# Kernel tuning notes

Measured on AMD Instinct MI355X. Metric: run time of the kernel, lower is better.

Reference implementation:

```python
import jax, jax.numpy as jnp
import numpy as np
import math

D_MODEL = 1024
N_HEADS = 16
D_K = D_MODEL // N_HEADS
BSZ = 4
SEQ = 2048


def setup_inputs() -> dict:
    key = jax.random.key(0)
    ks = jax.random.split(key, 10)
    x = jax.random.normal(ks[0], (BSZ, SEQ, D_MODEL), dtype=jnp.float32)
    pad_mask = jnp.zeros((BSZ, 1, 1, SEQ), dtype=jnp.int32)
    s = 0.02
    Wq = jax.random.normal(ks[1], (D_MODEL, D_MODEL), jnp.float32) * s
    bq = jax.random.normal(ks[2], (D_MODEL,), jnp.float32) * s
    Wk = jax.random.normal(ks[3], (D_MODEL, D_MODEL), jnp.float32) * s
    bk = jax.random.normal(ks[4], (D_MODEL,), jnp.float32) * s
    Wv = jax.random.normal(ks[5], (D_MODEL, D_MODEL), jnp.float32) * s
    bv = jax.random.normal(ks[6], (D_MODEL,), jnp.float32) * s
    Wo = jax.random.normal(ks[7], (D_MODEL, D_MODEL), jnp.float32) * s
    bo = jax.random.normal(ks[8], (D_MODEL,), jnp.float32) * s
    return {"x": x, "pad_mask": pad_mask, "Wq": Wq, "bq": bq, "Wk": Wk,
            "bk": bk, "Wv": Wv, "bv": bv, "Wo": Wo, "bo": bo}


def reference(x, pad_mask, Wq, bq, Wk, bk, Wv, bv, Wo, bo):
    bsz, seq_len, d_model = x.shape
    h, dk = N_HEADS, D_K

    def split(W, b):
        # torch Linear: x @ W.T + b ; then [b,s,h,dk] -> [b,h,s,dk]
        y = jnp.einsum('bsd,ed->bse', x, W) + b
        return y.reshape(bsz, seq_len, h, dk).transpose(0, 2, 1, 3)

    q = split(Wq, bq)
    k = split(Wk, bk)
    v = split(Wv, bv)

    scores = jnp.einsum('bhqd,bhkd->bhqk', q, k) / math.sqrt(dk)
    causal = jnp.triu(jnp.ones((seq_len, seq_len), dtype=bool), k=1)
    scores = jnp.where(causal[None, None], -jnp.inf, scores)
    scores = jnp.where(pad_mask == 1, -jnp.inf, scores)
    attn = jax.nn.softmax(scores, axis=-1)
    attn = jnp.nan_to_num(attn, nan=0.0)
    out = jnp.einsum('bhqk,bhkd->bhqd', attn, v)
    out = out.transpose(0, 2, 1, 3).reshape(bsz, seq_len, d_model)
    # dropout is identity in eval mode
    return jnp.einsum('bsd,ed->bse', out, Wo) + bo
```

## Files before the change

kernel.cpp:

```cpp
#include <hip/hip_runtime.h>
#include <stdint.h>
#include <stddef.h>


typedef __bf16 bf16;
typedef __bf16 bf16x8 __attribute__((ext_vector_type(8)));
typedef __bf16 bf16x4 __attribute__((ext_vector_type(4)));
typedef float f32x4 __attribute__((ext_vector_type(4)));

#define DM   1024
#define NH   16
#define DK   64
#define BSZ  4
#define SEQL 2048
#define NTOK 8192
#define NEGB -3.0e38f

__device__ __forceinline__ void async16(const bf16* g, void* l) {
  __builtin_amdgcn_global_load_lds(
      (__attribute__((address_space(1))) void*)g,
      (__attribute__((address_space(3))) void*)l, 16, 0, 0);
}

__global__ __launch_bounds__(256) void cvt_all(
    const float* __restrict__ x,
    const float* __restrict__ w0, const float* __restrict__ w1,
    const float* __restrict__ w2, const float* __restrict__ w3,
    const int* __restrict__ pad,
    bf16* __restrict__ xd,
    bf16* __restrict__ d0, bf16* __restrict__ d1,
    bf16* __restrict__ d2, bf16* __restrict__ d3,
    float* __restrict__ padf) {
  int blk = blockIdx.x;
  if (blk >= 6144) {
    int i = (blk - 6144) * 2048 + threadIdx.x * 8;
    int4 p0 = *(const int4*)(pad + i);
    int4 p1 = *(const int4*)(pad + i + 4);
    float4 o0 = {p0.x ? NEGB : 0.f, p0.y ? NEGB : 0.f, p0.z ? NEGB : 0.f, p0.w ? NEGB : 0.f};
    float4 o1 = {p1.x ? NEGB : 0.f, p1.y ? NEGB : 0.f, p1.z ? NEGB : 0.f, p1.w ? NEGB : 0.f};
    *(float4*)(padf + i) = o0;
    *(float4*)(padf + i + 4) = o1;
    return;
  }
  const float* s; bf16* d; int i;
  if (blk < 4096) { s = x; d = xd; i = blk * 2048 + threadIdx.x * 8; }
  else {
    int m = (blk - 4096) >> 9, bi = (blk - 4096) & 511;
    switch (m) {
      case 0:  s = w0; d = d0; break;
      case 1:  s = w1; d = d1; break;
      case 2:  s = w2; d = d2; break;
      default: s = w3; d = d3; break;
    }
    i = bi * 2048 + threadIdx.x * 8;
  }
  float4 v0 = *(const float4*)(s + i);
  float4 v1 = *(const float4*)(s + i + 4);
  bf16x8 o = {(bf16)v0.x, (bf16)v0.y, (bf16)v0.z, (bf16)v0.w,
              (bf16)v1.x, (bf16)v1.y, (bf16)v1.z, (bf16)v1.w};
  *(bf16x8*)(d + i) = o;
}

template <int OUT_MODE>
__device__ __forceinline__ void gemm_fine(const bf16* __restrict__ A,
                                          const bf16* __restrict__ W,
                                          const float* __restrict__ bias,
                                          void* __restrict__ outp,
                                          int bm, int bn, char* smem) {
  const int tid  = threadIdx.x;
  const int lane = tid & 63;
  const int wv   = tid >> 6;
  const int wr   = wv >> 2;
  const int wc   = wv & 3;
  const int c    = lane & 15;
  const int quad = lane >> 4;

  char* Ab = smem;
  char* Bb = smem + 24576;

  const int sr  = tid >> 2;
  const int sjj = ((tid & 3) ^ (sr & 3)) * 8;
  const bf16* gA = A + (size_t)(bm + sr) * DM + sjj;
  const bf16* gB = W + (size_t)(bn + sr) * DM + sjj;

#define STG(KT, U) {                                                     \
    async16(gA + (size_t)(KT) * 32, Ab + (U) * 8192 + tid * 16);         \
    async16(gB + (size_t)(KT) * 32, Bb + (U) * 16384 + tid * 16);        \
    async16(gB + (size_t)(KT) * 32 + (size_t)128 * DM,                   \
            Bb + (U) * 16384 + 8192 + tid * 16); }

  const int sw = (quad ^ (c & 3)) * 16;
  int aoff[4], boff[4];
#pragma unroll
  for (int i = 0; i < 4; ++i) {
    aoff[i] = (wr * 64 + i * 16 + c) * 64 + sw;
    boff[i] = (wc * 64 + i * 16 + c) * 64 + sw;
  }

  f32x4 acc[4][4] = {};

  STG(0, 0) STG(1, 1)
  asm volatile("s_waitcnt vmcnt(3)" ::: "memory");
  __builtin_amdgcn_s_barrier();
  __builtin_amdgcn_sched_barrier(0);

#pragma unroll
  for (int kt = 0; kt < 32; ++kt) {
    const char* Ac = Ab + (kt % 3) * 8192;
    const char* Bc = Bb + (kt % 3) * 16384;
    bf16x8 a[4], b[4];
#pragma unroll
    for (int i = 0; i < 4; ++i) a[i] = *(const bf16x8*)(Ac + aoff[i]);
#pragma unroll
    for (int i = 0; i < 4; ++i) b[i] = *(const bf16x8*)(Bc + boff[i]);
    if (kt + 2 < 32) STG(kt + 2, (kt + 2) % 3)
    __builtin_amdgcn_s_barrier();
    asm volatile("s_waitcnt lgkmcnt(0)" ::: "memory");
    __builtin_amdgcn_sched_barrier(0);
    __builtin_amdgcn_s_setprio(1);
#pragma unroll
    for (int mi = 0; mi < 4; ++mi)
#pragma unroll
      for (int ni = 0; ni < 4; ++ni)
        acc[mi][ni] = __builtin_amdgcn_mfma_f32_16x16x32_bf16(a[mi], b[ni],
                                                              acc[mi][ni], 0, 0, 0);
    __builtin_amdgcn_s_setprio(0);
    if (kt <= 29)      asm volatile("s_waitcnt vmcnt(3)" ::: "memory");
    else if (kt == 30) asm volatile("s_waitcnt vmcnt(0)" ::: "memory");
    if (kt != 31) {
      __builtin_amdgcn_s_barrier();
      __builtin_amdgcn_sched_barrier(0);
    }
  }
#undef STG

  float bias_r[4];
#pragma unroll
  for (int ni = 0; ni < 4; ++ni) bias_r[ni] = bias[bn + wc * 64 + ni * 16 + c];

  if constexpr (OUT_MODE == 2) {
    __syncthreads();
    bf16* vt = (bf16*)smem + wv * 4608;
#pragma unroll
    for (int mi = 0; mi < 4; ++mi)
#pragma unroll
      for (int ni = 0; ni < 4; ++ni) {
        bf16x4 pv = {(bf16)(acc[mi][ni][0] + bias_r[ni]),
                     (bf16)(acc[mi][ni][1] + bias_r[ni]),
                     (bf16)(acc[mi][ni][2] + bias_r[ni]),
                     (bf16)(acc[mi][ni][3] + bias_r[ni])};
        *(bf16x4*)&vt[(ni * 16 + c) * 72 + mi * 16 + quad * 4] = pv;
      }
    const int base = bm + wr * 64;
    const int bb = base >> 11, s0 = base & 2047;
    const int rl = lane >> 3, cl = lane & 7;
#pragma unroll
    for (int it = 0; it < 8; ++it) {
      int d_row = it * 8 + rl;
      bf16x8 v = *(const bf16x8*)&vt[d_row * 72 + cl * 8];
      int n_g = bn + wc * 64 + d_row;
      int hh = n_g >> 6, dd = n_g & 63;
      *(bf16x8*)&((bf16*)outp)[(((size_t)(bb * NH + hh)) * DK + dd) * SEQL + s0 + cl * 8] = v;
    }
    return;
  }

#pragma unroll
  for (int mi = 0; mi < 4; ++mi) {
#pragma unroll
    for (int reg = 0; reg < 4; ++reg) {
      int m_g = bm + wr * 64 + mi * 16 + quad * 4 + reg;
#pragma unroll
      for (int ni = 0; ni < 4; ++ni) {
        int n_g = bn + wc * 64 + ni * 16 + c;
        float v = acc[mi][ni][reg] + bias_r[ni];
        if constexpr (OUT_MODE == 0) {
          int b = m_g >> 11, s = m_g & 2047;
          int h = n_g >> 6, d = n_g & 63;
          ((bf16*)outp)[(((size_t)(b * NH + h) * SEQL + s) << 6) + d] = (bf16)v;
        } else {
          ((float*)outp)[(size_t)m_g * DM + n_g] = v;
        }
      }
    }
  }
}

__global__ __launch_bounds__(512, 4) void qkv_gemm(
    const bf16* __restrict__ X,
    const bf16* __restrict__ Wq, const bf16* __restrict__ Wk, const bf16* __restrict__ Wv,
    const float* __restrict__ bq, const float* __restrict__ bk, const float* __restrict__ bv,
    bf16* __restrict__ Q, bf16* __restrict__ K, bf16* __restrict__ Vt) {
  __shared__ alignas(16) char smem[73728];
  const int f   = blockIdx.x;
  const int xcd = f & 7;
  const int c96 = f >> 3;
  const int z   = c96 >> 5;
  const int r   = c96 & 31;
  const int bm  = (xcd * 8 + (r >> 2)) * 128;
  const int bn  = (r & 3) * 256;
  if (z == 0)      gemm_fine<0>(X, Wq, bq, Q,  bm, bn, smem);
  else if (z == 1) gemm_fine<0>(X, Wk, bk, K,  bm, bn, smem);
  else             gemm_fine<2>(X, Wv, bv, Vt, bm, bn, smem);
}

__global__ __launch_bounds__(512, 4) void out_gemm(const bf16* __restrict__ A,
                                                   const bf16* __restrict__ W,
                                                   const float* __restrict__ bias,
                                                   float* __restrict__ out) {
  __shared__ alignas(16) char smem[73728];
  const int f   = blockIdx.x;
  const int c32 = f >> 3;
  const int bm  = ((f & 7) * 8 + (c32 >> 2)) * 128;
  const int bn  = (c32 & 3) * 256;
  gemm_fine<1>(A, W, bias, out, bm, bn, smem);
}

__global__ __launch_bounds__(512, 2) void attn_kernel(
    const bf16* __restrict__ Q, const bf16* __restrict__ K,
    const bf16* __restrict__ Vt, const float* __restrict__ padf,
    bf16* __restrict__ O) {
  const int B = blockIdx.x;
  const int bh = (B & 7) + 8 * (B >> 5);
  const int t  = (B >> 3) & 3;
  const int b = bh >> 4, h = bh & 15;
  const int tid  = threadIdx.x;
  const int lane = tid & 63;
  const int wv   = tid >> 6;
  const int c    = lane & 15;
  const int quad = lane >> 4;

  __shared__ bf16 Ks[2][64 * 64];
  __shared__ bf16 Vs[2][64 * 64];
  __shared__ bf16 Pl_all[8][32 * 64];
  bf16* Pl = &Pl_all[wv][0];

  const bf16* Qh  = Q  + (size_t)bh * SEQL * DK;
  const bf16* Kh  = K  + (size_t)bh * SEQL * DK;
  const bf16* Vth = Vt + (size_t)bh * DK * SEQL;
  const float* pb = padf + b * SEQL;

  const int sr = tid >> 3;
  const int sj = ((tid & 7) ^ (sr & 7)) * 8;
  const bf16* gK = Kh  + (size_t)sr * DK   + sj;
  const bf16* gV = Vth + (size_t)sr * SEQL + sj;
  bf16* lK0 = &Ks[0][tid * 8]; bf16* lK1 = &Ks[1][tid * 8];
  bf16* lV0 = &Vs[0][tid * 8]; bf16* lV1 = &Vs[1][tid * 8];

  const float sc = 0.1803368801111204f;

  for (int pass = 0; pass < 2; ++pass) {
    const int qt  = pass ? 7 - t : t;
    const int R   = qt * 256 + wv * 32;
    const int nkt = (qt + 1) * 4;

    bf16x8 Qf[2][2];
#pragma unroll
    for (int qg = 0; qg < 2; ++qg)
#pragma unroll
      for (int kh = 0; kh < 2; ++kh)
        Qf[qg][kh] = *(const bf16x8*)&Qh[(size_t)(R + qg * 16 + c) * DK + kh * 32 + quad * 8];

    f32x4 Oc[2][4] = {};
    float ls[2] = {0.f, 0.f};

    __syncthreads();
    async16(gK, lK0);
    async16(gV, lV0);

    for (int kt = 0; kt < nkt; ++kt) {
      const int cur = kt & 1;
      const int kb = kt * 64;
      __syncthreads();

      if (kt + 1 < nkt) {
        async16(gK + (size_t)(kt + 1) * 64 * DK, cur ? lK0 : lK1);
        async16(gV + (size_t)(kt + 1) * 64,      cur ? lV0 : lV1);
      }
      if (kb > R + 31) continue;

      float4 bc[4];
#pragma unroll
      for (int kf = 0; kf < 4; ++kf)
        bc[kf] = *(const float4*)&pb[kb + kf * 16 + quad * 4];

      const bf16* Kc = cur ? Ks[1] : Ks[0];
      const bf16* Vc = cur ? Vs[1] : Vs[0];

      bf16x8 Kf[4][2], Vf[4][2];
#pragma unroll
      for (int kf = 0; kf < 4; ++kf)
#pragma unroll
        for (int kh = 0; kh < 2; ++kh)
          Kf[kf][kh] = *(const bf16x8*)&Kc[(kf * 16 + c) * 64 + (((kh * 4 + quad) ^ (c & 7)) * 8)];
#pragma unroll
      for (int df = 0; df < 4; ++df)
#pragma unroll
        for (int kv = 0; kv < 2; ++kv)
          Vf[df][kv] = *(const bf16x8*)&Vc[(df * 16 + c) * 64 + (((kv * 4 + quad) ^ (c & 7)) * 8)];

      f32x4 st[2][4] = {};
#pragma unroll
      for (int qg = 0; qg < 2; ++qg)
#pragma unroll
        for (int kh = 0; kh < 2; ++kh)
#pragma unroll
          for (int kf = 0; kf < 4; ++kf)
            st[qg][kf] = __builtin_amdgcn_mfma_f32_16x16x32_bf16(Kf[kf][kh], Qf[qg][kh],
                                                                 st[qg][kf], 0, 0, 0);

      const bool dg = (kb + 63 > R);
#pragma unroll
      for (int qg = 0; qg < 2; ++qg) {
        const int qrow = R + qg * 16 + c;
#pragma unroll
        for (int kf = 0; kf < 4; ++kf) {
          const float* bv4 = (const float*)&bc[kf];
          float p4[4];
#pragma unroll
          for (int r = 0; r < 4; ++r) {
            float e = __builtin_amdgcn_exp2f(__builtin_fmaf(st[qg][kf][r], sc, bv4[r]));
            if (dg && (kb + kf * 16 + quad * 4 + r > qrow)) e = 0.f;
            p4[r] = e;
            ls[qg] += e;
          }
          bf16x4 pk = {(bf16)p4[0], (bf16)p4[1], (bf16)p4[2], (bf16)p4[3]};
          *(bf16x4*)&Pl[(qg * 16 + c) * 64 +
                        (((kf * 2 + (quad >> 1)) ^ (c & 7)) * 8) + (quad & 1) * 4] = pk;
        }
      }

#pragma unroll
      for (int qg = 0; qg < 2; ++qg)
#pragma unroll
        for (int kv = 0; kv < 2; ++kv) {
          bf16x8 af = *(const bf16x8*)&Pl[(qg * 16 + c) * 64 +
                                          (((kv * 4 + quad) ^ (c & 7)) * 8)];
#pragma unroll
          for (int df = 0; df < 4; ++df)
            Oc[qg][df] = __builtin_amdgcn_mfma_f32_16x16x32_bf16(af, Vf[df][kv],
                                                                 Oc[qg][df], 0, 0, 0);
        }
    }

#pragma unroll
    for (int qg = 0; qg < 2; ++qg) {
      float l = ls[qg];
      l += __shfl_xor(l, 16);
      l += __shfl_xor(l, 32);
      float linv = (l > 0.f) ? 1.f / l : 0.f;
      float lr[4];
#pragma unroll
      for (int r = 0; r < 4; ++r) lr[r] = __shfl(linv, quad * 4 + r);
#pragma unroll
      for (int r = 0; r < 4; ++r) {
        size_t row = (size_t)(b * SEQL + R + qg * 16 + quad * 4 + r) * DM + h * DK;
#pragma unroll
        for (int df = 0; df < 4; ++df)
          O[row + df * 16 + c] = (bf16)(Oc[qg][df][r] * lr[r]);
      }
    }
  }
}

extern "C" void kernel_launch(void* const* d_in, const int* in_sizes, int n_in,
                              void* d_out, int out_size, void* d_ws, size_t ws_size,
                              hipStream_t stream) {
  const float* x   = (const float*)d_in[0];
  const int*   pad = (const int*)d_in[1];
  const float* Wq  = (const float*)d_in[2];
  const float* bq  = (const float*)d_in[3];
  const float* Wk  = (const float*)d_in[4];
  const float* bk  = (const float*)d_in[5];
  const float* Wv  = (const float*)d_in[6];
  const float* bv  = (const float*)d_in[7];
  const float* Wo  = (const float*)d_in[8];
  const float* bo  = (const float*)d_in[9];
  float* out = (float*)d_out;

  const size_t SZ_X = (size_t)NTOK * DM * 2;
  const size_t SZ_W = (size_t)DM * DM * 2;
  char* ws = (char*)d_ws;
  bf16* Xb  = (bf16*)ws;  ws += SZ_X;
  bf16* Wqb = (bf16*)ws;  ws += SZ_W;
  bf16* Wkb = (bf16*)ws;  ws += SZ_W;
  bf16* Wvb = (bf16*)ws;  ws += SZ_W;
  bf16* Wob = (bf16*)ws;  ws += SZ_W;
  bf16* Qb  = (bf16*)ws;  ws += SZ_X;
  bf16* Kb  = (bf16*)ws;  ws += SZ_X;
  bf16* Vtb = (bf16*)ws;  ws += SZ_X;
  bf16* Ob  = (bf16*)ws;  ws += SZ_X;
  float* padfb = (float*)ws; ws += (size_t)NTOK * 4;

  cvt_all<<<6148, 256, 0, stream>>>(x, Wq, Wk, Wv, Wo, pad,
                                    Xb, Wqb, Wkb, Wvb, Wob, padfb);
  qkv_gemm<<<768, 512, 0, stream>>>(Xb, Wqb, Wkb, Wvb, bq, bk, bv, Qb, Kb, Vtb);
  attn_kernel<<<256, 512, 0, stream>>>(Qb, Kb, Vtb, padfb, Ob);
  out_gemm<<<256, 512, 0, stream>>>(Ob, Wob, bo, out);
}
```

Measured before the change: 235.0 us.

## Halve attention block size to 128 rows and compute row sums via MFMA

The attention kernel now runs 512 blocks of 256 threads, each handling 128-row query tiles (16 tiles per head, paired for causal load balance), instead of 256 blocks of 512 threads with 256-row tiles. Each thread issues two async loads per K/V tile to fill the shared buffers. The softmax denominator is computed by an extra MFMA of P against a ones vector, which replaces per-element scalar accumulation and cross-lane shuffles. The intent is better occupancy and finer causal load balance, at the cost of more blocks each re-streaming K/V and one extra MFMA per P chunk.

```diff
diff --git a/kernel.cpp b/kernel.cpp
--- a/kernel.cpp
+++ b/kernel.cpp
@@ -216,13 +216,15 @@
   gemm_fine<1>(A, W, bias, out, bm, bn, smem);
 }
 
-__global__ __launch_bounds__(512, 2) void attn_kernel(
+__global__ __launch_bounds__(256, 2) void attn_kernel(
     const bf16* __restrict__ Q, const bf16* __restrict__ K,
     const bf16* __restrict__ Vt, const float* __restrict__ padf,
     bf16* __restrict__ O) {
   const int B = blockIdx.x;
-  const int bh = (B & 7) + 8 * (B >> 5);
-  const int t  = (B >> 3) & 3;
+  const int xcd = B & 7;
+  const int g = B >> 3;
+  const int bh = xcd + 8 * (g >> 3);
+  const int t = g & 7;
   const int b = bh >> 4, h = bh & 15;
   const int tid  = threadIdx.x;
   const int lane = tid & 63;
@@ -232,7 +234,7 @@
 
   __shared__ bf16 Ks[2][64 * 64];
   __shared__ bf16 Vs[2][64 * 64];
-  __shared__ bf16 Pl_all[8][32 * 64];
+  __shared__ bf16 Pl_all[4][32 * 64];
   bf16* Pl = &Pl_all[wv][0];
 
   const bf16* Qh  = Q  + (size_t)bh * SEQL * DK;
@@ -244,15 +246,19 @@
   const int sj = ((tid & 7) ^ (sr & 7)) * 8;
   const bf16* gK = Kh  + (size_t)sr * DK   + sj;
   const bf16* gV = Vth + (size_t)sr * SEQL + sj;
-  bf16* lK0 = &Ks[0][tid * 8]; bf16* lK1 = &Ks[1][tid * 8];
-  bf16* lV0 = &Vs[0][tid * 8]; bf16* lV1 = &Vs[1][tid * 8];
-
+  bf16* lK[2] = {&Ks[0][tid * 8], &Ks[1][tid * 8]};
+  bf16* lV[2] = {&Vs[0][tid * 8], &Vs[1][tid * 8]};
+  bf16* lKb[2] = {&Ks[0][(tid + 256) * 8], &Ks[1][(tid + 256) * 8]};
+  bf16* lVb[2] = {&Vs[0][(tid + 256) * 8], &Vs[1][(tid + 256) * 8]};
+
+  const bf16 one1 = (bf16)1.f;
+  const bf16x8 ones = {one1, one1, one1, one1, one1, one1, one1, one1};
   const float sc = 0.1803368801111204f;
 
   for (int pass = 0; pass < 2; ++pass) {
-    const int qt  = pass ? 7 - t : t;
-    const int R   = qt * 256 + wv * 32;
-    const int nkt = (qt + 1) * 4;
+    const int qt  = pass ? 15 - t : t;
+    const int R   = qt * 128 + wv * 32;
+    const int nkt = 2 * (qt + 1);
 
     bf16x8 Qf[2][2];
 #pragma unroll
@@ -262,11 +268,13 @@
         Qf[qg][kh] = *(const bf16x8*)&Qh[(size_t)(R + qg * 16 + c) * DK + kh * 32 + quad * 8];
 
     f32x4 Oc[2][4] = {};
-    float ls[2] = {0.f, 0.f};
+    f32x4 Oc1[2] = {};
 
     __syncthreads();
-    async16(gK, lK0);
-    async16(gV, lV0);
+    async16(gK, lK[0]);
+    async16(gK + (size_t)32 * DK, lKb[0]);
+    async16(gV, lV[0]);
+    async16(gV + (size_t)32 * SEQL, lVb[0]);
 
     for (int kt = 0; kt < nkt; ++kt) {
       const int cur = kt & 1;
@@ -274,8 +282,12 @@
       __syncthreads();
 
       if (kt + 1 < nkt) {
-        async16(gK + (size_t)(kt + 1) * 64 * DK, cur ? lK0 : lK1);
-        async16(gV + (size_t)(kt + 1) * 64,      cur ? lV0 : lV1);
+        const bf16* gKn = gK + (size_t)(kt + 1) * 64 * DK;
+        const bf16* gVn = gV + (size_t)(kt + 1) * 64;
+        async16(gKn, lK[cur ^ 1]);
+        async16(gKn + (size_t)32 * DK, lKb[cur ^ 1]);
+        async16(gVn, lV[cur ^ 1]);
+        async16(gVn + (size_t)32 * SEQL, lVb[cur ^ 1]);
       }
       if (kb > R + 31) continue;
 
@@ -284,8 +296,8 @@
       for (int kf = 0; kf < 4; ++kf)
         bc[kf] = *(const float4*)&pb[kb + kf * 16 + quad * 4];
 
-      const bf16* Kc = cur ? Ks[1] : Ks[0];
-      const bf16* Vc = cur ? Vs[1] : Vs[0];
+      const bf16* Kc = Ks[cur];
+      const bf16* Vc = Vs[cur];
 
       bf16x8 Kf[4][2], Vf[4][2];
 #pragma unroll
@@ -322,7 +334,6 @@
             float e = __builtin_amdgcn_exp2f(__builtin_fmaf(st[qg][kf][r], sc, bv4[r]));
             if (dg && (kb + kf * 16 + quad * 4 + r > qrow)) e = 0.f;
             p4[r] = e;
-            ls[qg] += e;
           }
           bf16x4 pk = {(bf16)p4[0], (bf16)p4[1], (bf16)p4[2], (bf16)p4[3]};
           *(bf16x4*)&Pl[(qg * 16 + c) * 64 +
@@ -340,24 +351,20 @@
           for (int df = 0; df < 4; ++df)
             Oc[qg][df] = __builtin_amdgcn_mfma_f32_16x16x32_bf16(af, Vf[df][kv],
                                                                  Oc[qg][df], 0, 0, 0);
+          Oc1[qg] = __builtin_amdgcn_mfma_f32_16x16x32_bf16(af, ones, Oc1[qg], 0, 0, 0);
         }
     }
 
 #pragma unroll
     for (int qg = 0; qg < 2; ++qg) {
-      float l = ls[qg];
-      l += __shfl_xor(l, 16);
-      l += __shfl_xor(l, 32);
-      float linv = (l > 0.f) ? 1.f / l : 0.f;
-      float lr[4];
-#pragma unroll
-      for (int r = 0; r < 4; ++r) lr[r] = __shfl(linv, quad * 4 + r);
 #pragma unroll
       for (int r = 0; r < 4; ++r) {
+        float l = Oc1[qg][r];
+        float linv = (l > 0.f) ? 1.f / l : 0.f;
         size_t row = (size_t)(b * SEQL + R + qg * 16 + quad * 4 + r) * DM + h * DK;
 #pragma unroll
         for (int df = 0; df < 4; ++df)
-          O[row + df * 16 + c] = (bf16)(Oc[qg][df][r] * lr[r]);
+          O[row + df * 16 + c] = (bf16)(Oc[qg][df][r] * linv);
       }
     }
   }
@@ -395,6 +402,6 @@
   cvt_all<<<6148, 256, 0, stream>>>(x, Wq, Wk, Wv, Wo, pad,
                                     Xb, Wqb, Wkb, Wvb, Wob, padfb);
   qkv_gemm<<<768, 512, 0, stream>>>(Xb, Wqb, Wkb, Wvb, bq, bk, bv, Qb, Kb, Vtb);
-  attn_kernel<<<256, 512, 0, stream>>>(Qb, Kb, Vtb, padfb, Ob);
+  attn_kernel<<<512, 256, 0, stream>>>(Qb, Kb, Vtb, padfb, Ob);
   out_gemm<<<256, 512, 0, stream>>>(Ob, Wob, bo, out);
 }
```

Measured after the change: 240.6 us. +2.4%, slower.
